# Optimization experiments

Hardware: AMD Instinct MI355X
Metric: run time of the kernel (lower is better)

## Reference

```python
import jax, jax.numpy as jnp
import numpy as np

IN_F, H, T, NUM_CLASSES, WINDOW_HALF = 14, 24, 25, 4, 12


def _lstm_dir(x_tbf, w_ih, w_hh, b_ih, b_hh, reverse):
    # x_tbf: [T,B,F]; w_ih: [4H,F]; w_hh: [4H,H]; biases: [4H]
    B = x_tbf.shape[1]
    xw = jnp.einsum('tbf,gf->tbg', x_tbf, w_ih) + b_ih + b_hh  # [T,B,4H]

    def step(carry, xw_t):
        h, c = carry
        gates = xw_t + h @ w_hh.T
        i, f, g, o = jnp.split(gates, 4, axis=-1)
        i, f, o = jax.nn.sigmoid(i), jax.nn.sigmoid(f), jax.nn.sigmoid(o)
        g = jnp.tanh(g)
        c = f * c + i * g
        h = o * jnp.tanh(c)
        return (h, c), h

    h0 = jnp.zeros((B, H), x_tbf.dtype)
    c0 = jnp.zeros((B, H), x_tbf.dtype)
    _, hs = jax.lax.scan(step, (h0, c0), xw, reverse=reverse)
    return hs  # [T,B,H], in original time order


def setup_inputs() -> dict:
    key = jax.random.key(0)
    ks = jax.random.split(key, 12)
    s_ih = 1.0 / np.sqrt(H)
    u = lambda k, shape: jax.random.uniform(k, shape, jnp.float32, -s_ih, s_ih)
    return {
        'x': jax.random.normal(ks[0], (65536, T, IN_F), jnp.float32),
        'w_ih_f': u(ks[1], (4 * H, IN_F)),
        'w_hh_f': u(ks[2], (4 * H, H)),
        'b_ih_f': u(ks[3], (4 * H,)),
        'b_hh_f': u(ks[4], (4 * H,)),
        'w_ih_b': u(ks[5], (4 * H, IN_F)),
        'w_hh_b': u(ks[6], (4 * H, H)),
        'b_ih_b': u(ks[7], (4 * H,)),
        'b_hh_b': u(ks[8], (4 * H,)),
        'head_w': u(ks[9], (NUM_CLASSES, 2 * H)),
        'head_b': u(ks[10], (NUM_CLASSES,)),
    }


def reference(x, w_ih_f, w_hh_f, b_ih_f, b_hh_f, w_ih_b, w_hh_b, b_ih_b, b_hh_b, head_w, head_b):
    x_tbf = jnp.transpose(x, (1, 0, 2))  # [T,B,F]
    h_f = _lstm_dir(x_tbf, w_ih_f, w_hh_f, b_ih_f, b_hh_f, reverse=False)
    h_b = _lstm_dir(x_tbf, w_ih_b, w_hh_b, b_ih_b, b_hh_b, reverse=True)
    center = jnp.concatenate([h_f[WINDOW_HALF], h_b[WINDOW_HALF]], axis=-1)  # [B,2H]
    # dropout is identity in eval mode
    return center @ head_w.T + head_b  # [B,4]
```

## Files before the change

kernel.cpp:

```cpp
#include <hip/hip_runtime.h>

typedef __attribute__((ext_vector_type(8))) short frag8;
typedef __attribute__((ext_vector_type(4))) float f4;
typedef __attribute__((ext_vector_type(4))) unsigned int u4;
typedef __attribute__((ext_vector_type(2))) float f2;

namespace {
constexpr int T_STEPS = 25;
constexpr int IN_F    = 14;
constexpr int H       = 24;
constexpr int NSTEP   = 13;
constexpr int WAVE_LDS = NSTEP * 1024;
constexpr float LOG2E    = 1.4426950408889634f;
constexpr float TWOLOG2E = 2.8853900817779268f;
}

#if __has_builtin(__builtin_amdgcn_exp2f)
#define EXP2F(v) __builtin_amdgcn_exp2f(v)
#else
#define EXP2F(v) __expf(0.6931471805599453f * (v))
#endif

__device__ __forceinline__ unsigned short bf16_rne(float f) {
    unsigned int u = __float_as_uint(f);
    u += 0x7fff + ((u >> 16) & 1);
    return (unsigned short)(u >> 16);
}
__device__ __forceinline__ float bf16_to_f(unsigned short s) {
    return __uint_as_float(((unsigned int)s) << 16);
}
__device__ __forceinline__ float fast_rcp(float x) { return __builtin_amdgcn_rcpf(x); }

__global__ void pack_mfma(const float* __restrict__ wif, const float* __restrict__ whf,
                          const float* __restrict__ bif, const float* __restrict__ bhf,
                          const float* __restrict__ wib, const float* __restrict__ whb,
                          const float* __restrict__ bib, const float* __restrict__ bhb,
                          unsigned short* __restrict__ ws)
{
    const int gid = blockIdx.x * 256 + threadIdx.x;
    if (gid >= 2048) return;
    const int lane = gid & 63;
    const int tile = (gid >> 6) & 7;
    const int set  = (gid >> 9) & 1;
    const int dir  = (gid >> 10) & 1;
    const int n = lane & 15, q = lane >> 4;
    const int r = tile * 16 + n;
    const int g = r >> 5, u_row = r & 31;
    const bool vrow = (u_row < 24);
    const float* Wx = dir ? wib : wif;
    const float* Wh = dir ? whb : whf;
    const float* bi = dir ? bib : bif;
    const float* bh = dir ? bhb : bhf;
    const int rowW = g * 24 + (vrow ? u_row : 0);
    const float scale = (g == 2) ? TWOLOG2E : -LOG2E;
    unsigned short vals[8];
    #pragma unroll
    for (int j = 0; j < 8; ++j) {
        const int k = q * 8 + j;
        unsigned short o = 0;
        if (vrow) {
            if (set == 0) {
                if (k < 28) {
                    const int f = (k < 14) ? k : k - 14;
                    o = bf16_rne(scale * Wx[rowW * IN_F + f]);
                } else if (k < 30) {
                    const float b = scale * (bi[rowW] + bh[rowW]);
                    const unsigned short hi = bf16_rne(b);
                    o = (k == 28) ? hi : bf16_rne(b - bf16_to_f(hi));
                }
            } else {
                const int j7 = k & 7, kq = k >> 3;
                const int uh = (j7 < 4) ? kq * 4 + j7 : 16 + kq * 4 + (j7 - 4);
                if (uh < 24) o = bf16_rne(scale * Wh[rowW * H + uh]);
            }
        }
        vals[j] = o;
    }
    unsigned short* d = ws + (size_t)gid * 8;
    #pragma unroll
    for (int j = 0; j < 8; ++j) d[j] = vals[j];
}

__global__ __launch_bounds__(128, 3)
void bilstm_mfma(const float* __restrict__ x, const unsigned short* __restrict__ wpk,
                 const float* __restrict__ head_w, const float* __restrict__ head_b,
                 float* __restrict__ out, int B)
{
    __align__(16) __shared__ unsigned char arena[2 * WAVE_LDS];

    const int tid  = threadIdx.x;
    const int wave = __builtin_amdgcn_readfirstlane(tid >> 6);
    const int lane = tid & 63;
    const int q    = lane >> 4;
    const int col  = lane & 15;
    const int b0   = blockIdx.x * 16;

    frag8 Aw[2][8];
    #pragma unroll
    for (int s = 0; s < 2; ++s)
        #pragma unroll
        for (int t = 0; t < 8; ++t)
            Aw[s][t] = ((const frag8*)wpk)[((wave * 2 + s) * 8 + t) * 64 + lane];

    unsigned char* xbase = arena + wave * WAVE_LDS;

    auto stage_x = [&](int si, int e) {
        const int t = wave ? (T_STEPS - 1 - si) : si;
        const float* xr = x + ((size_t)(b0 + e) * T_STEPS + t) * IN_F;
        unsigned int xu[IN_F];
        #pragma unroll
        for (int i = 0; i < 7; ++i) {
            f2 v = *(const f2*)(xr + 2 * i);
            xu[2*i] = __float_as_uint(v.x); xu[2*i+1] = __float_as_uint(v.y);
        }
        unsigned int lo[IN_F];
        #pragma unroll
        for (int i = 0; i < IN_F; ++i)
            lo[i] = __float_as_uint(__uint_as_float(xu[i])
                                    - __uint_as_float(xu[i] & 0xFFFF0000u));
        unsigned int w[16];
        #pragma unroll
        for (int i = 0; i < 7; ++i)
            w[i] = __builtin_amdgcn_perm(xu[2*i+1], xu[2*i], 0x07060302u);
        w[7] = __builtin_amdgcn_perm(lo[1], lo[0], 0x07060302u);
        #pragma unroll
        for (int i = 0; i < 6; ++i)
            w[8 + i] = __builtin_amdgcn_perm(lo[2*i+3], lo[2*i+2], 0x07060302u);
        w[14] = 0x3F803F80u;
        w[15] = 0u;
        #pragma unroll
        for (int qq = 0; qq < 4; ++qq)
            *(u4*)(xbase + si * 1024 + qq * 256 + e * 16) =
                (u4){w[qq*4], w[qq*4+1], w[qq*4+2], w[qq*4+3]};
    };

    for (int rr = lane; rr < NSTEP * 16; rr += 64) stage_x(rr >> 4, rr & 15);

    float c_st[2][4];
    #pragma unroll
    for (int p = 0; p < 2; ++p)
        #pragma unroll
        for (int r = 0; r < 4; ++r) c_st[p][r] = 0.0f;

    float hv[2][4];
    frag8 Bhh, Bhl;
    const f4 zc = {0.f, 0.f, 0.f, 0.f};

    const unsigned char* xrd = xbase + q * 256 + col * 16;

    auto gates = [&](f4* acc) {
        float hl[2][4];
        #pragma unroll
        for (int p = 0; p < 2; ++p) {
            #pragma unroll
            for (int r = 0; r < 4; ++r) {
                const float ig = fast_rcp(1.0f + EXP2F(acc[0 + p][r]));
                const float fg = fast_rcp(1.0f + EXP2F(acc[2 + p][r]));
                const float gg = 1.0f - 2.0f * fast_rcp(1.0f + EXP2F(acc[4 + p][r]));
                const float og = fast_rcp(1.0f + EXP2F(acc[6 + p][r]));
                const float cn = fg * c_st[p][r] + ig * gg;
                c_st[p][r] = cn;
                const float tc = 1.0f - 2.0f * fast_rcp(1.0f + EXP2F(TWOLOG2E * cn));
                const float h  = og * tc;
                hv[p][r] = h;
                hl[p][r] = h - __uint_as_float(__float_as_uint(h) & 0xFFFF0000u);
            }
        }
        const u4 uh4 = {
            __builtin_amdgcn_perm(__float_as_uint(hv[0][1]), __float_as_uint(hv[0][0]), 0x07060302u),
            __builtin_amdgcn_perm(__float_as_uint(hv[0][3]), __float_as_uint(hv[0][2]), 0x07060302u),
            __builtin_amdgcn_perm(__float_as_uint(hv[1][1]), __float_as_uint(hv[1][0]), 0x07060302u),
            __builtin_amdgcn_perm(__float_as_uint(hv[1][3]), __float_as_uint(hv[1][2]), 0x07060302u)};
        const u4 ul4 = {
            __builtin_amdgcn_perm(__float_as_uint(hl[0][1]), __float_as_uint(hl[0][0]), 0x07060302u),
            __builtin_amdgcn_perm(__float_as_uint(hl[0][3]), __float_as_uint(hl[0][2]), 0x07060302u),
            __builtin_amdgcn_perm(__float_as_uint(hl[1][1]), __float_as_uint(hl[1][0]), 0x07060302u),
            __builtin_amdgcn_perm(__float_as_uint(hl[1][3]), __float_as_uint(hl[1][2]), 0x07060302u)};
        Bhh = __builtin_bit_cast(frag8, uh4);
        Bhl = __builtin_bit_cast(frag8, ul4);
    };

    {
        const frag8 Bx = *(const frag8*)(xrd);
        f4 acc[8];
        #pragma unroll
        for (int t = 0; t < 8; ++t)
            acc[t] = __builtin_amdgcn_mfma_f32_16x16x32_bf16(Aw[0][t], Bx, zc, 0, 0, 0);
        gates(acc);
    }

    #pragma unroll 1
    for (int s = 1; s < NSTEP; ++s) {
        const frag8 Bx = *(const frag8*)(xrd + s * 1024);
        f4 acc[8];
        #pragma unroll
        for (int t = 0; t < 8; ++t) {
            acc[t] = __builtin_amdgcn_mfma_f32_16x16x32_bf16(Aw[0][t], Bx,  zc,     0, 0, 0);
            acc[t] = __builtin_amdgcn_mfma_f32_16x16x32_bf16(Aw[1][t], Bhh, acc[t], 0, 0, 0);
            acc[t] = __builtin_amdgcn_mfma_f32_16x16x32_bf16(Aw[1][t], Bhl, acc[t], 0, 0, 0);
        }
        gates(acc);
    }

    *(f4*)(xbase + col * 96 + q * 16) = (f4){hv[0][0], hv[0][1], hv[0][2], hv[0][3]};
    if (q < 2)
        *(f4*)(xbase + col * 96 + 64 + q * 16) = (f4){hv[1][0], hv[1][1], hv[1][2], hv[1][3]};

    __syncthreads();

    if (tid < 64) {
        const int e = tid >> 2, cls = tid & 3;
        float acc = head_b[cls];
        const float* hf = (const float*)(arena + e * 96);
        const float* hb = (const float*)(arena + WAVE_LDS + e * 96);
        #pragma unroll
        for (int u = 0; u < H; ++u)
            acc += hf[u] * head_w[cls * 2 * H + u] + hb[u] * head_w[cls * 2 * H + H + u];
        out[(size_t)b0 * 4 + tid] = acc;
    }
}

extern "C" void kernel_launch(void* const* d_in, const int* in_sizes, int n_in,
                              void* d_out, int out_size, void* d_ws, size_t ws_size,
                              hipStream_t stream)
{
    const float* x      = (const float*)d_in[0];
    const float* w_ih_f = (const float*)d_in[1];
    const float* w_hh_f = (const float*)d_in[2];
    const float* b_ih_f = (const float*)d_in[3];
    const float* b_hh_f = (const float*)d_in[4];
    const float* w_ih_b = (const float*)d_in[5];
    const float* w_hh_b = (const float*)d_in[6];
    const float* b_ih_b = (const float*)d_in[7];
    const float* b_hh_b = (const float*)d_in[8];
    const float* head_w = (const float*)d_in[9];
    const float* head_b = (const float*)d_in[10];
    float* out = (float*)d_out;
    unsigned short* ws = (unsigned short*)d_ws;

    const int B = in_sizes[0] / (T_STEPS * IN_F);

    hipLaunchKernelGGL(pack_mfma, dim3(8), dim3(256), 0, stream,
                       w_ih_f, w_hh_f, b_ih_f, b_hh_f,
                       w_ih_b, w_hh_b, b_ih_b, b_hh_b, ws);
    hipLaunchKernelGGL(bilstm_mfma, dim3((B + 15) / 16), dim3(128), 0, stream,
                       x, ws, head_w, head_b, out, B);
}
```

Measured before the change: 198.0 us.

## Repack gate rows into six MFMA tiles and merge sigmoid reciprocals

The gate weights are repacked from 8 padded 16-row tiles (32 rows per gate, 8 of them padding) into 6 tiles. The first four tiles hold hidden units 0-15 for each gate, and the last two interleave all four gates for units 16-23. This cuts MFMAs per step from 24 to 18 and removes wasted padding work. The gate math is also rewritten algebraically so that the sigmoid and tanh reciprocals are combined into fewer rcp calls per cell. The cost is extra multiplies, a more intricate fragment layout for the hidden-state B operand, and some added numeric risk from the products of exponentials.

New measurement: 177.8 us. 10.2% less time.

```diff
diff --git a/kernel.cpp b/kernel.cpp
--- a/kernel.cpp
+++ b/kernel.cpp
@@ -38,41 +38,41 @@
                           unsigned short* __restrict__ ws)
 {
     const int gid = blockIdx.x * 256 + threadIdx.x;
-    if (gid >= 2048) return;
+    if (gid >= 1536) return;
     const int lane = gid & 63;
-    const int tile = (gid >> 6) & 7;
-    const int set  = (gid >> 9) & 1;
-    const int dir  = (gid >> 10) & 1;
-    const int n = lane & 15, q = lane >> 4;
-    const int r = tile * 16 + n;
-    const int g = r >> 5, u_row = r & 31;
-    const bool vrow = (u_row < 24);
+    const int tile = (gid >> 6) % 6;
+    const int set  = (gid / 384) & 1;
+    const int dir  = gid / 768;
+    const int m = lane & 15, q = lane >> 4;
+    const int g = (tile < 4) ? tile : (m & 3);
+    const int u_row = (tile < 4) ? m : ((tile == 4 ? 16 : 20) + (m >> 2));
     const float* Wx = dir ? wib : wif;
     const float* Wh = dir ? whb : whf;
     const float* bi = dir ? bib : bif;
     const float* bh = dir ? bhb : bhf;
-    const int rowW = g * 24 + (vrow ? u_row : 0);
+    const int rowW = g * 24 + u_row;
     const float scale = (g == 2) ? TWOLOG2E : -LOG2E;
     unsigned short vals[8];
     #pragma unroll
     for (int j = 0; j < 8; ++j) {
         const int k = q * 8 + j;
         unsigned short o = 0;
-        if (vrow) {
-            if (set == 0) {
-                if (k < 28) {
-                    const int f = (k < 14) ? k : k - 14;
-                    o = bf16_rne(scale * Wx[rowW * IN_F + f]);
-                } else if (k < 30) {
-                    const float b = scale * (bi[rowW] + bh[rowW]);
-                    const unsigned short hi = bf16_rne(b);
-                    o = (k == 28) ? hi : bf16_rne(b - bf16_to_f(hi));
-                }
-            } else {
-                const int j7 = k & 7, kq = k >> 3;
-                const int uh = (j7 < 4) ? kq * 4 + j7 : 16 + kq * 4 + (j7 - 4);
-                if (uh < 24) o = bf16_rne(scale * Wh[rowW * H + uh]);
+        if (set == 0) {
+            if (k < 28) {
+                const int f = (k < 14) ? k : k - 14;
+                o = bf16_rne(scale * Wx[rowW * IN_F + f]);
+            } else if (k < 30) {
+                const float b = scale * (bi[rowW] + bh[rowW]);
+                const unsigned short hi = bf16_rne(b);
+                o = (k == 28) ? hi : bf16_rne(b - bf16_to_f(hi));
             }
+        } else {
+            const int j7 = k & 7, kq = k >> 3;
+            int uh = -1;
+            if (j7 < 4)       uh = kq * 4 + j7;
+            else if (j7 == 4) uh = 16 + kq;
+            else if (j7 == 5) uh = 20 + kq;
+            if (uh >= 0) o = bf16_rne(scale * Wh[rowW * H + uh]);
         }
         vals[j] = o;
     }
@@ -95,12 +95,12 @@
     const int col  = lane & 15;
     const int b0   = blockIdx.x * 16;
 
-    frag8 Aw[2][8];
+    frag8 Aw[2][6];
     #pragma unroll
     for (int s = 0; s < 2; ++s)
         #pragma unroll
-        for (int t = 0; t < 8; ++t)
-            Aw[s][t] = ((const frag8*)wpk)[((wave * 2 + s) * 8 + t) * 64 + lane];
+        for (int t = 0; t < 6; ++t)
+            Aw[s][t] = ((const frag8*)wpk)[((wave * 2 + s) * 6 + t) * 64 + lane];
 
     unsigned char* xbase = arena + wave * WAVE_LDS;
 
@@ -136,55 +136,77 @@
 
     for (int rr = lane; rr < NSTEP * 16; rr += 64) stage_x(rr >> 4, rr & 15);
 
-    float c_st[2][4];
-    #pragma unroll
-    for (int p = 0; p < 2; ++p)
-        #pragma unroll
-        for (int r = 0; r < 4; ++r) c_st[p][r] = 0.0f;
-
-    float hv[2][4];
+    f4    cv = {0.f, 0.f, 0.f, 0.f};
+    float c_s[2] = {0.f, 0.f};
+    f4    Hv;
+    float h_s[2];
     frag8 Bhh, Bhl;
     const f4 zc = {0.f, 0.f, 0.f, 0.f};
 
     const unsigned char* xrd = xbase + q * 256 + col * 16;
 
-    auto gates = [&](f4* acc) {
-        float hl[2][4];
-        #pragma unroll
-        for (int p = 0; p < 2; ++p) {
-            #pragma unroll
-            for (int r = 0; r < 4; ++r) {
-                const float ig = fast_rcp(1.0f + EXP2F(acc[0 + p][r]));
-                const float fg = fast_rcp(1.0f + EXP2F(acc[2 + p][r]));
-                const float gg = 1.0f - 2.0f * fast_rcp(1.0f + EXP2F(acc[4 + p][r]));
-                const float og = fast_rcp(1.0f + EXP2F(acc[6 + p][r]));
-                const float cn = fg * c_st[p][r] + ig * gg;
-                c_st[p][r] = cn;
-                const float tc = 1.0f - 2.0f * fast_rcp(1.0f + EXP2F(TWOLOG2E * cn));
-                const float h  = og * tc;
-                hv[p][r] = h;
-                hl[p][r] = h - __uint_as_float(__float_as_uint(h) & 0xFFFF0000u);
-            }
-        }
+    auto gates = [&](const f4* acc) {
+        f4 EI, EF, EG, EO, EC;
+        #pragma unroll
+        for (int r = 0; r < 4; ++r) {
+            EI[r] = EXP2F(acc[0][r]);
+            EF[r] = EXP2F(acc[1][r]);
+            EG[r] = EXP2F(acc[2][r]);
+            EO[r] = EXP2F(acc[3][r]);
+        }
+        const f4 P  = (EI + 1.0f) * (EG + 1.0f);
+        const f4 Df = P * (EF + 1.0f);
+        f4 Rf;
+        #pragma unroll
+        for (int r = 0; r < 4; ++r) Rf[r] = fast_rcp(Df[r]);
+        cv = (cv * P + (EG - 1.0f) * (EF + 1.0f)) * Rf;
+        #pragma unroll
+        for (int r = 0; r < 4; ++r) EC[r] = EXP2F(TWOLOG2E * cv[r]);
+        const f4 Do = (EO + 1.0f) * (EC + 1.0f);
+        f4 Ro;
+        #pragma unroll
+        for (int r = 0; r < 4; ++r) Ro[r] = fast_rcp(Do[r]);
+        Hv = (EC - 1.0f) * Ro;
+
+        #pragma unroll
+        for (int s = 0; s < 2; ++s) {
+            const float ei = EXP2F(acc[4 + s][0]);
+            const float ef = EXP2F(acc[4 + s][1]);
+            const float eg = EXP2F(acc[4 + s][2]);
+            const float eo = EXP2F(acc[4 + s][3]);
+            const float P2 = (1.0f + ei) * (1.0f + eg);
+            const float cn = (c_s[s] * P2 + (eg - 1.0f) * (1.0f + ef))
+                             * fast_rcp(P2 * (1.0f + ef));
+            c_s[s] = cn;
+            const float ec = EXP2F(TWOLOG2E * cn);
+            h_s[s] = (ec - 1.0f) * fast_rcp((1.0f + eo) * (1.0f + ec));
+        }
+
+        f4 Hl;
+        #pragma unroll
+        for (int r = 0; r < 4; ++r)
+            Hl[r] = Hv[r] - __uint_as_float(__float_as_uint(Hv[r]) & 0xFFFF0000u);
+        const float hl4 = h_s[0] - __uint_as_float(__float_as_uint(h_s[0]) & 0xFFFF0000u);
+        const float hl5 = h_s[1] - __uint_as_float(__float_as_uint(h_s[1]) & 0xFFFF0000u);
         const u4 uh4 = {
-            __builtin_amdgcn_perm(__float_as_uint(hv[0][1]), __float_as_uint(hv[0][0]), 0x07060302u),
-            __builtin_amdgcn_perm(__float_as_uint(hv[0][3]), __float_as_uint(hv[0][2]), 0x07060302u),
-            __builtin_amdgcn_perm(__float_as_uint(hv[1][1]), __float_as_uint(hv[1][0]), 0x07060302u),
-            __builtin_amdgcn_perm(__float_as_uint(hv[1][3]), __float_as_uint(hv[1][2]), 0x07060302u)};
+            __builtin_amdgcn_perm(__float_as_uint(Hv[1]), __float_as_uint(Hv[0]), 0x07060302u),
+            __builtin_amdgcn_perm(__float_as_uint(Hv[3]), __float_as_uint(Hv[2]), 0x07060302u),
+            __builtin_amdgcn_perm(__float_as_uint(h_s[1]), __float_as_uint(h_s[0]), 0x07060302u),
+            0u};
         const u4 ul4 = {
-            __builtin_amdgcn_perm(__float_as_uint(hl[0][1]), __float_as_uint(hl[0][0]), 0x07060302u),
-            __builtin_amdgcn_perm(__float_as_uint(hl[0][3]), __float_as_uint(hl[0][2]), 0x07060302u),
-            __builtin_amdgcn_perm(__float_as_uint(hl[1][1]), __float_as_uint(hl[1][0]), 0x07060302u),
-            __builtin_amdgcn_perm(__float_as_uint(hl[1][3]), __float_as_uint(hl[1][2]), 0x07060302u)};
+            __builtin_amdgcn_perm(__float_as_uint(Hl[1]), __float_as_uint(Hl[0]), 0x07060302u),
+            __builtin_amdgcn_perm(__float_as_uint(Hl[3]), __float_as_uint(Hl[2]), 0x07060302u),
+            __builtin_amdgcn_perm(__float_as_uint(hl5), __float_as_uint(hl4), 0x07060302u),
+            0u};
         Bhh = __builtin_bit_cast(frag8, uh4);
         Bhl = __builtin_bit_cast(frag8, ul4);
     };
 
     {
         const frag8 Bx = *(const frag8*)(xrd);
-        f4 acc[8];
-        #pragma unroll
-        for (int t = 0; t < 8; ++t)
+        f4 acc[6];
+        #pragma unroll
+        for (int t = 0; t < 6; ++t)
             acc[t] = __builtin_amdgcn_mfma_f32_16x16x32_bf16(Aw[0][t], Bx, zc, 0, 0, 0);
         gates(acc);
     }
@@ -192,9 +214,9 @@
     #pragma unroll 1
     for (int s = 1; s < NSTEP; ++s) {
         const frag8 Bx = *(const frag8*)(xrd + s * 1024);
-        f4 acc[8];
-        #pragma unroll
-        for (int t = 0; t < 8; ++t) {
+        f4 acc[6];
+        #pragma unroll
+        for (int t = 0; t < 6; ++t) {
             acc[t] = __builtin_amdgcn_mfma_f32_16x16x32_bf16(Aw[0][t], Bx,  zc,     0, 0, 0);
             acc[t] = __builtin_amdgcn_mfma_f32_16x16x32_bf16(Aw[1][t], Bhh, acc[t], 0, 0, 0);
             acc[t] = __builtin_amdgcn_mfma_f32_16x16x32_bf16(Aw[1][t], Bhl, acc[t], 0, 0, 0);
@@ -202,9 +224,9 @@
         gates(acc);
     }
 
-    *(f4*)(xbase + col * 96 + q * 16) = (f4){hv[0][0], hv[0][1], hv[0][2], hv[0][3]};
-    if (q < 2)
-        *(f4*)(xbase + col * 96 + 64 + q * 16) = (f4){hv[1][0], hv[1][1], hv[1][2], hv[1][3]};
+    *(f4*)(xbase + col * 96 + q * 16) = Hv;
+    *(float*)(xbase + col * 96 + 64 + q * 4) = h_s[0];
+    *(float*)(xbase + col * 96 + 80 + q * 4) = h_s[1];
 
     __syncthreads();
 
@@ -240,7 +262,7 @@
 
     const int B = in_sizes[0] / (T_STEPS * IN_F);
 
-    hipLaunchKernelGGL(pack_mfma, dim3(8), dim3(256), 0, stream,
+    hipLaunchKernelGGL(pack_mfma, dim3(6), dim3(256), 0, stream,
                        w_ih_f, w_hh_f, b_ih_f, b_hh_f,
                        w_ih_b, w_hh_b, b_ih_b, b_hh_b, ws);
     hipLaunchKernelGGL(bilstm_mfma, dim3((B + 15) / 16), dim3(128), 0, stream,
```
